# Performance work log

Hardware: AMD Instinct MI355X
Metric: run time of the kernel (lower is better)

## Reference

```python
import jax, jax.numpy as jnp
import numpy as np

B, L, D = 16, 1024, 512
MAX_LEN = 1024  # module hardcodes self.max_len = 1024


def setup_inputs() -> dict:
    key = jax.random.key(0)
    k0, k1, k2, k3, k4 = jax.random.split(key, 5)
    s = 1.0 / np.sqrt(D)
    return {
        "x": jax.random.normal(k0, (B, L, D), jnp.float32),
        "generator": 0.02 * jax.random.normal(k1, (D, 2 * MAX_LEN - 1), jnp.float32),
        "Wq": jax.random.normal(k2, (D, D), jnp.float32) * s,
        "Wv": jax.random.normal(k3, (D, D), jnp.float32) * s,
        "Wc": jax.random.normal(k4, (D, D), jnp.float32) * s,
    }


def reference(x, generator, Wq, Wv, Wc):
    Bc, Lc, Dc = x.shape
    q = x @ Wq.T                      # (B, L, D)
    v = x @ Wv.T                      # (B, L, D)
    # extract_center_window: window of size 2L-1 centered at MAX_LEN-1
    center_full = (generator.shape[-1] + 1) // 2  # == MAX_LEN
    gen = generator[:, center_full - Lc: center_full + Lc - 1]  # (D, 2L-1)
    w = jnp.einsum('bld,di->bli', q, gen)  # (B, L, 2L-1)
    # Toeplitz gather: out[b, l, i] = w[b, l, (L-1) - l + i]
    r = jnp.arange(Lc)
    idx = (Lc - 1) - r[:, None] + r[None, :]  # (L, L)
    w = jnp.take_along_axis(w, idx[None, :, :], axis=-1)  # (B, L, L)
    w = jnp.cumsum(w, axis=1)
    w = jax.nn.relu(w)
    w = jnp.tril(w)
    w = w / (jnp.sum(w, axis=-1, keepdims=True) + 1e-8)
    out = jnp.einsum('bli,bid->bld', w, v)  # (B, L, D)
    return out @ Wc.T
```

## Files before the change

kernel.cpp:

```cpp
#include <hip/hip_runtime.h>
#include <hip/hip_bf16.h>

typedef __attribute__((ext_vector_type(8))) __bf16 bf16x8;
typedef __attribute__((ext_vector_type(4))) __bf16 bf16x4;
typedef __attribute__((ext_vector_type(4))) float  f32x4;

__device__ __forceinline__ void gl_lds16(const __bf16* g, __bf16* l) {
  __builtin_amdgcn_global_load_lds(
      (const __attribute__((address_space(1))) void*)g,
      (__attribute__((address_space(3))) void*)l,
      16, 0, 0);
}


__global__ __launch_bounds__(256) void prep_kernel(
    const float* __restrict__ x, const float* __restrict__ gen,
    const float* __restrict__ Wq, const float* __restrict__ Wv, const float* __restrict__ Wc,
    __bf16* __restrict__ xb, __bf16* __restrict__ genT,
    __bf16* __restrict__ wqT, __bf16* __restrict__ wvT, __bf16* __restrict__ wcb,
    float* __restrict__ gp) {
  __shared__ float S[64][65];
  const int blk = blockIdx.x, tid = threadIdx.x;

  if (blk < 128) {
    const float* in = (blk < 64) ? Wq : Wv;
    __bf16* out = (blk < 64) ? wqT : wvT;
    int t = blk & 63;
    int tx = tid & 63, ty = tid >> 6;
    int d0 = (t >> 3) * 64, e0 = (t & 7) * 64;
#pragma unroll
    for (int i = 0; i < 16; ++i) {
      int di = i * 4 + ty;
      S[di][tx] = in[(long)(d0 + di) * 512 + e0 + tx];
    }
    __syncthreads();
#pragma unroll
    for (int i = 0; i < 16; ++i) {
      int ei = i * 4 + ty;
      out[(long)(e0 + ei) * 512 + d0 + tx] = (__bf16)S[tx][ei];
    }
  } else if (blk < 384) {
    int i = (blk - 128) * 256 + tid;
    float4 v = ((const float4*)Wc)[i];
    bf16x4 o;
    o[0] = (__bf16)v.x; o[1] = (__bf16)v.y; o[2] = (__bf16)v.z; o[3] = (__bf16)v.w;
    *(bf16x4*)(wcb + 4L * i) = o;
  } else if (blk < 2432) {
    int i = blk - 384;
    for (int d = tid; d < 512; d += 256) {
      float v = (i < 2047) ? gen[(long)d * 2047 + i] : 0.f;
      genT[(long)i * 512 + d] = (__bf16)v;
    }
  } else if (blk < 10624) {
    int i = (blk - 2432) * 256 + tid;
    float4 v = ((const float4*)x)[i];
    bf16x4 o;
    o[0] = (__bf16)v.x; o[1] = (__bf16)v.y; o[2] = (__bf16)v.z; o[3] = (__bf16)v.w;
    *(bf16x4*)(xb + 4L * i) = o;
  } else {
    int t = blk - 10624;
    int i = t % 63, c = t / 63;
    int d0 = c * 64, k = tid;
    float a0 = 0.f, a1 = 0.f;
#pragma unroll 8
    for (int u = 0; u < 64; ++u) {
      int d = d0 + u;
      float g = gen[(long)d * 2047 + 992 + i];
      a0 += Wq[(long)d * 512 + k] * g;
      a1 += Wq[(long)d * 512 + k + 256] * g;
    }
    long o = ((long)c * 63 + i) * 512;
    gp[o + k] = a0;
    gp[o + k + 256] = a1;
  }
}

__device__ __forceinline__ void gemm128_body(
    const __bf16* __restrict__ Ab, const __bf16* __restrict__ Bb,
    __bf16 (*As)[128 * 32], __bf16 (*Bs)[128 * 32],
    int m0, int n0, int K, int nt, f32x4 (&acc)[4][4]) {
  const int tid = threadIdx.x;
  const int w = tid >> 6, l = tid & 63;
  const int srow = w * 16 + (l >> 2);
  const int scol = (((l & 3) ^ ((l >> 3) & 3))) * 8;
  const int wr = (w >> 1) * 64, wc = (w & 1) * 64;
  const int fr = l & 15;
  const int cp = (((l >> 4) ^ ((fr >> 1) & 3))) << 3;

  auto STAGE = [&](int t, int p) {
    const int k0 = t << 5;
    gl_lds16(Ab + (long)(m0 + srow) * K + (k0 + scol),      &As[p][(w * 16) * 32]);
    gl_lds16(Ab + (long)(m0 + 64 + srow) * K + (k0 + scol), &As[p][(64 + w * 16) * 32]);
    gl_lds16(Bb + (long)(n0 + srow) * K + (k0 + scol),      &Bs[p][(w * 16) * 32]);
    gl_lds16(Bb + (long)(n0 + 64 + srow) * K + (k0 + scol), &Bs[p][(64 + w * 16) * 32]);
  };
  STAGE(0, 0);
  if (nt > 1) STAGE(1, 1);
  if (nt > 2) STAGE(2, 2);
  int p = 0;
  for (int t = 0; t < nt; ++t) {
    const int ahead = nt - 1 - t;
    if (ahead >= 2)      asm volatile("s_waitcnt vmcnt(8)\ns_barrier" ::: "memory");
    else if (ahead == 1) asm volatile("s_waitcnt vmcnt(4)\ns_barrier" ::: "memory");
    else                 asm volatile("s_waitcnt vmcnt(0)\ns_barrier" ::: "memory");
    bf16x8 af[4], bg[4];
#pragma unroll
    for (int i = 0; i < 4; ++i) af[i] = *(const bf16x8*)&As[p][(wr + i * 16 + fr) * 32 + cp];
#pragma unroll
    for (int j = 0; j < 4; ++j) bg[j] = *(const bf16x8*)&Bs[p][(wc + j * 16 + fr) * 32 + cp];
    asm volatile("s_waitcnt lgkmcnt(0)\ns_barrier" ::: "memory");
    if (t + 3 < nt) STAGE(t + 3, p);
#pragma unroll
    for (int i = 0; i < 4; ++i)
#pragma unroll
      for (int j = 0; j < 4; ++j)
        acc[i][j] = __builtin_amdgcn_mfma_f32_16x16x32_bf16(af[i], bg[j], acc[i][j], 0, 0, 0);
    p = (p == 2) ? 0 : p + 1;
  }
}

__global__ __launch_bounds__(256) void gemm_fold(
    const __bf16* __restrict__ A1, const __bf16* __restrict__ B1, __bf16* __restrict__ C1,
    const __bf16* __restrict__ A2, const __bf16* __restrict__ B2, __bf16* __restrict__ C2,
    const float* __restrict__ gp, float* __restrict__ g2t) {
  __shared__ __bf16 As[3][128 * 32];
  __shared__ __bf16 Bs[3][128 * 32];
  const int b = blockIdx.x;
  if (b >= 80) {
    int idx = (b - 80) * 256 + threadIdx.x;
    if (idx >= 63 * 512) return;
    float s = 0.f;
#pragma unroll
    for (int c = 0; c < 8; ++c) s += gp[(long)c * 63 * 512 + idx];
    g2t[idx] = s;
    return;
  }
  const __bf16 *Ab, *Bb; __bf16* C; int m0, n0;
  if (b < 16) { Ab = A1; Bb = B1; C = C1; m0 = (b >> 2) * 128; n0 = (b & 3) * 128; }
  else { int t = b - 16; Ab = A2; Bb = B2; C = C2; m0 = (t >> 2) * 128; n0 = (t & 3) * 128; }

  f32x4 acc[4][4] = {};
  gemm128_body(Ab, Bb, As, Bs, m0, n0, 512, 16, acc);

  const int l = threadIdx.x & 63, w = threadIdx.x >> 6;
  const int rbase = m0 + (w >> 1) * 64 + ((l >> 4) << 2);
  const int cbase = n0 + (w & 1) * 64 + (l & 15);
#pragma unroll
  for (int i = 0; i < 4; ++i)
#pragma unroll
    for (int r = 0; r < 4; ++r) {
      long row = rbase + i * 16 + r;
#pragma unroll
      for (int j = 0; j < 4; ++j) C[row * 512 + cbase + j * 16] = (__bf16)acc[i][j][r];
    }
}

__global__ __launch_bounds__(256) void gemm_out(
    const __bf16* __restrict__ A, const __bf16* __restrict__ B, float* __restrict__ Cv,
    const float* __restrict__ aux) {
  __shared__ __bf16 As[3][128 * 32];
  __shared__ __bf16 Bs[3][128 * 32];
  int bid = blockIdx.x;
  int swz = (bid & 7) * 64 + (bid >> 3);
  int xn = swz & 3, tt = swz >> 2;
  int yn = tt & 7, bz = tt >> 3;
  const int m0 = yn * 128, n0 = xn * 128;
  const int K = 1024;
  const __bf16* Ab = A + (long)bz * 1024 * 1024;
  const __bf16* Bb = B + (long)bz * 512 * 1024;
  const int nt = (m0 + 128) >> 5;

  f32x4 acc[4][4] = {};
  gemm128_body(Ab, Bb, As, Bs, m0, n0, K, nt, acc);

  const int l = threadIdx.x & 63, w = threadIdx.x >> 6;
  const int rbase = m0 + (w >> 1) * 64 + ((l >> 4) << 2);
  const int cbase = n0 + (w & 1) * 64 + (l & 15);
  float* C = Cv + (long)bz * 512 * 1024;
  const float* ax = aux + bz * 1024;
#pragma unroll
  for (int i = 0; i < 4; ++i)
#pragma unroll
    for (int r = 0; r < 4; ++r) {
      long row = rbase + i * 16 + r;
      float sc = 1.f / (ax[row] + 1e-8f);
#pragma unroll
      for (int j = 0; j < 4; ++j) C[row * 512 + cbase + j * 16] = acc[i][j][r] * sc;
    }
}

__global__ __launch_bounds__(512) void gemm_x(
    const __bf16* __restrict__ A, const __bf16* __restrict__ Bg,
    const __bf16* __restrict__ Pm, __bf16* __restrict__ S, __bf16* __restrict__ vT) {
  __shared__ __bf16 As[3][256 * 32];
  __shared__ __bf16 Bs[3][128 * 32];
  const int tid = threadIdx.x;
  const int w = tid >> 6, l = tid & 63;

  int wgid = blockIdx.x;
  int swz = (wgid & 7) * 112 + (wgid >> 3);
  int y = swz / 14, xt = swz - y * 14;
  const bool band = (xt < 10);
  const int m0 = y * 256;
  const int n0 = band ? (6 - 2 * (y & 3) + xt) * 128 : (xt - 10) * 128;
  const __bf16* Bb = band ? Bg : Pm;
  const int K = 512;

  const int srow = w * 16 + (l >> 2);
  const int scol = (((l & 3) ^ ((l >> 3) & 3))) * 8;
  const int wr = (w >> 1) * 64;
  const int wc = (w & 1) * 64;
  const int fr = l & 15;
  const int cp = (((l >> 4) ^ ((fr >> 1) & 3))) << 3;

  f32x4 acc[4][4] = {};

  auto STAGE = [&](int t, int p) {
    const int k0 = t << 5;
    gl_lds16(A + (long)(m0 + srow) * K + (k0 + scol),        &As[p][(w * 16) * 32]);
    gl_lds16(A + (long)(m0 + 128 + srow) * K + (k0 + scol),  &As[p][(128 + w * 16) * 32]);
    gl_lds16(Bb + (long)(n0 + srow) * K + (k0 + scol),       &Bs[p][(w * 16) * 32]);
  };

  STAGE(0, 0);
  STAGE(1, 1);
  STAGE(2, 2);

  int p = 0;
  for (int t = 0; t < 16; ++t) {
    const int ahead = 15 - t;
    if (ahead >= 2)      asm volatile("s_waitcnt vmcnt(6)\ns_barrier" ::: "memory");
    else if (ahead == 1) asm volatile("s_waitcnt vmcnt(3)\ns_barrier" ::: "memory");
    else                 asm volatile("s_waitcnt vmcnt(0)\ns_barrier" ::: "memory");
    bf16x8 af[4], bg[4];
#pragma unroll
    for (int i = 0; i < 4; ++i) af[i] = *(const bf16x8*)&As[p][(wr + i * 16 + fr) * 32 + cp];
#pragma unroll
    for (int j = 0; j < 4; ++j) bg[j] = *(const bf16x8*)&Bs[p][(wc + j * 16 + fr) * 32 + cp];
    asm volatile("s_waitcnt lgkmcnt(0)\ns_barrier" ::: "memory");
    if (t + 3 < 16) STAGE(t + 3, p);
#pragma unroll
    for (int i = 0; i < 4; ++i)
#pragma unroll
      for (int j = 0; j < 4; ++j)
        acc[i][j] = __builtin_amdgcn_mfma_f32_16x16x32_bf16(af[i], bg[j], acc[i][j], 0, 0, 0);
    p = (p == 2) ? 0 : p + 1;
  }

  const int rbase = m0 + wr + ((l >> 4) << 2);
  const int cbase = n0 + wc + fr;

  if (band) {
#pragma unroll
    for (int i = 0; i < 4; ++i)
#pragma unroll
      for (int r = 0; r < 4; ++r) {
        int row = rbase + i * 16 + r;
        int lloc = row & 1023;
#pragma unroll
        for (int j = 0; j < 4; ++j) {
          int jj = cbase + j * 16 - 1023 + lloc;
          if ((unsigned)jj < 1024u)
            S[(long)row * 1024 + jj] = (__bf16)acc[i][j][r];
        }
      }
  } else {
#pragma unroll
    for (int i = 0; i < 4; ++i) {
      int gm = rbase + i * 16;
      int bt = gm >> 10, lloc = gm & 1023;
#pragma unroll
      for (int j = 0; j < 4; ++j) {
        bf16x4 pk;
        pk[0] = (__bf16)acc[i][j][0]; pk[1] = (__bf16)acc[i][j][1];
        pk[2] = (__bf16)acc[i][j][2]; pk[3] = (__bf16)acc[i][j][3];
        *(bf16x4*)&vT[((long)bt * 512 + cbase + j * 16) * 1024 + lloc] = pk;
      }
    }
  }
}

__global__ __launch_bounds__(128) void chunk_sums(const __bf16* __restrict__ S,
                                                  float* __restrict__ csum,
                                                  float* __restrict__ rowsum) {
  int j0 = threadIdx.x * 8;
  int c = blockIdx.x, b = blockIdx.y;
  if (c < 8) rowsum[b * 1024 + c * 128 + threadIdx.x] = 0.f;
  const __bf16* Sb = S + (long)b * 1024 * 1024;
  float a[8] = {};
  int l0 = c * 16;
  for (int l = l0; l < l0 + 16; ++l) {
    bf16x8 v = *(const bf16x8*)&Sb[(long)l * 1024 + j0];
#pragma unroll
    for (int k = 0; k < 8; ++k) a[k] += (float)v[k];
  }
  long o = ((long)(b * 64 + c) << 10) + j0;
#pragma unroll
  for (int k = 0; k < 8; ++k) csum[o + k] = a[k];
}

__global__ __launch_bounds__(256) void scan_dots(
    float* __restrict__ csum,
    const float* __restrict__ x, const float* __restrict__ g2t, float* __restrict__ Sg) {
  const int blk = blockIdx.x, tid = threadIdx.x;
  if (blk < 64) {
    int idx = blk * 256 + tid;
    int b = idx >> 10, j = idx & 1023;
    long base = ((long)b * 64 << 10) + j;
    float v[64];
#pragma unroll
    for (int c = 0; c < 64; ++c) v[c] = csum[base + ((long)c << 10)];
    float s = 0.f;
#pragma unroll
    for (int c = 0; c < 64; ++c) { csum[base + ((long)c << 10)] = s; s += v[c]; }
  } else {
    int gid = (blk - 64) * 4 + (tid >> 6);
    int lane = tid & 63;
    int b = gid >> 10, rem = gid & 1023, m = rem >> 5, j = rem & 31;
    const float4* xr = (const float4*)(x + ((long)b * 1024 + m) * 512);
    const float4* gr = (const float4*)(g2t + (long)(31 - m + j) * 512);
    float4 a0 = xr[lane * 2], a1 = xr[lane * 2 + 1];
    float4 c0 = gr[lane * 2], c1 = gr[lane * 2 + 1];
    float s = a0.x * c0.x + a0.y * c0.y + a0.z * c0.z + a0.w * c0.w
            + a1.x * c1.x + a1.y * c1.y + a1.z * c1.z + a1.w * c1.w;
#pragma unroll
    for (int off = 32; off; off >>= 1) s += __shfl_down(s, off);
    if (lane == 0) Sg[gid] = s;
  }
}

__global__ __launch_bounds__(128) void cumsum_relu(const __bf16* __restrict__ S,
                                                   const float* __restrict__ csum,
                                                   const float* __restrict__ Sx,
                                                   __bf16* __restrict__ wrelu,
                                                   float* __restrict__ rowsum) {
  int j0 = threadIdx.x * 8;
  int c = blockIdx.x, b = blockIdx.y;
  const bool exact = (c < 2) && (j0 < 32);
  float run[8];
  if (exact) {
#pragma unroll
    for (int k = 0; k < 8; ++k) run[k] = 0.f;
    for (int m = 0; m < c * 16; ++m)
#pragma unroll
      for (int k = 0; k < 8; ++k) run[k] += Sx[b * 1024 + m * 32 + j0 + k];
  } else {
    long co = ((long)(b * 64 + c) << 10) + j0;
#pragma unroll
    for (int k = 0; k < 8; ++k) run[k] = csum[co + k];
  }
  const __bf16* Sb = S + (long)b * 1024 * 1024;
  __bf16* wr = wrelu + (long)b * 1024 * 1024;
  int l0 = c * 16;
  for (int l = l0; l < l0 + 16; ++l) {
    bf16x8 o;
    float rs = 0.f;
    if (exact) {
#pragma unroll
      for (int k = 0; k < 8; ++k) {
        run[k] += Sx[b * 1024 + l * 32 + j0 + k];
        float val = (j0 + k <= l) ? fmaxf(run[k], 0.f) : 0.f;
        o[k] = (__bf16)val;
        rs += val;
      }
    } else {
      bf16x8 v = *(const bf16x8*)&Sb[(long)l * 1024 + j0];
#pragma unroll
      for (int k = 0; k < 8; ++k) {
        run[k] += (float)v[k];
        float val = (j0 + k <= l) ? fmaxf(run[k], 0.f) : 0.f;
        o[k] = (__bf16)val;
        rs += val;
      }
    }
    if (j0 < (((l >> 7) + 1) << 7))
      *(bf16x8*)&wr[(long)l * 1024 + j0] = o;
#pragma unroll
    for (int off = 32; off; off >>= 1) rs += __shfl_down(rs, off);
    if ((threadIdx.x & 63) == 0 && rs != 0.f) atomicAdd(&rowsum[b * 1024 + l], rs);
  }
}

extern "C" void kernel_launch(void* const* d_in, const int* in_sizes, int n_in,
                              void* d_out, int out_size, void* d_ws, size_t ws_size,
                              hipStream_t stream) {
  const float* x   = (const float*)d_in[0];
  const float* gen = (const float*)d_in[1];
  const float* Wq  = (const float*)d_in[2];
  const float* Wv  = (const float*)d_in[3];
  const float* Wc  = (const float*)d_in[4];

  char* ws = (char*)d_ws;
  __bf16* xb    = (__bf16*)(ws + 0L);
  __bf16* vT    = (__bf16*)(ws + 33554432L);
  __bf16* Smat  = (__bf16*)(ws + 67108864L);
  __bf16* wrelu = (__bf16*)(ws + 134217728L);
  __bf16* genT  = (__bf16*)(ws + 167772160L);
  __bf16* wqT   = (__bf16*)(ws + 169869312L);
  __bf16* wvT   = (__bf16*)(ws + 170393600L);
  __bf16* wcb   = (__bf16*)(ws + 170917888L);
  float*  g2t   = (float*)(ws + 171442176L);
  float*  csum  = (float*)(ws + 16777216L);
  float*  rsum  = (float*)(ws + 16777216L + 4194304L);
  float*  Sbuf  = (float*)(ws + 16777216L + 4259840L);
  __bf16* Pmat  = (__bf16*)(ws + 50331648L);
  __bf16* Bg    = (__bf16*)(ws + 51380224L);
  float*  gp    = (float*)(ws + 58720256L);

  prep_kernel<<<11128, 256, 0, stream>>>(x, gen, Wq, Wv, Wc, xb, genT, wqT, wvT, wcb, gp);

  gemm_fold<<<206, 256, 0, stream>>>(wcb, wvT, Pmat, genT, wqT, Bg, gp, g2t);

  gemm_x<<<896, 512, 0, stream>>>(xb, Bg, Pmat, Smat, vT);

  chunk_sums<<<dim3(64, 16), 128, 0, stream>>>(Smat, csum, rsum);
  scan_dots<<<4160, 256, 0, stream>>>(csum, x, g2t, Sbuf);
  cumsum_relu<<<dim3(64, 16), 128, 0, stream>>>(Smat, csum, Sbuf, wrelu, rsum);

  gemm_out<<<512, 256, 0, stream>>>(wrelu, vT, (float*)d_out, rsum);
}
```

Baseline: 137.8 us.

## Enlarge gemm_x tile to 256x256 with BK=64 double-buffered interleaved staging

Rewrites the gemm_x kernel to use 256x256 output tiles with a K-step of 64 and two LDS buffers instead of 256x128 tiles with K-step 32 and three buffers. The band/Toeplitz tile mapping is adjusted to match, so the grid shrinks from 896 to 448 workgroups. Global-to-LDS loads are split into half-tiles and interleaved with the MFMA sub-phases, and s_setprio is raised around the MFMA blocks. The aim is to raise arithmetic intensity and hide load latency. In exchange it uses much more LDS and more accumulator registers per thread, which lowers occupancy, and the band region may now compute more wasted tiles.

After: 139.3 us. Within noise of the previous version (+1.0%).

```diff
diff --git a/kernel.cpp b/kernel.cpp
--- a/kernel.cpp
+++ b/kernel.cpp
@@ -11,7 +11,6 @@
       (__attribute__((address_space(3))) void*)l,
       16, 0, 0);
 }
-
 
 __global__ __launch_bounds__(256) void prep_kernel(
     const float* __restrict__ x, const float* __restrict__ gen,
@@ -192,67 +191,108 @@
 __global__ __launch_bounds__(512) void gemm_x(
     const __bf16* __restrict__ A, const __bf16* __restrict__ Bg,
     const __bf16* __restrict__ Pm, __bf16* __restrict__ S, __bf16* __restrict__ vT) {
-  __shared__ __bf16 As[3][256 * 32];
-  __shared__ __bf16 Bs[3][128 * 32];
+  __shared__ __bf16 Al[2][256 * 64];
+  __shared__ __bf16 Bl[2][256 * 64];
   const int tid = threadIdx.x;
   const int w = tid >> 6, l = tid & 63;
 
   int wgid = blockIdx.x;
-  int swz = (wgid & 7) * 112 + (wgid >> 3);
-  int y = swz / 14, xt = swz - y * 14;
-  const bool band = (xt < 10);
+  int swz = (wgid & 7) * 56 + (wgid >> 3);
+  int y = swz / 7, xt = swz - y * 7;
+  const bool band = (xt < 5);
   const int m0 = y * 256;
-  const int n0 = band ? (6 - 2 * (y & 3) + xt) * 128 : (xt - 10) * 128;
+  const int n0 = band ? (3 - (y & 3) + xt) * 256 : (xt - 5) * 256;
   const __bf16* Bb = band ? Bg : Pm;
   const int K = 512;
 
-  const int srow = w * 16 + (l >> 2);
-  const int scol = (((l & 3) ^ ((l >> 3) & 3))) * 8;
-  const int wr = (w >> 1) * 64;
-  const int wc = (w & 1) * 64;
-  const int fr = l & 15;
-  const int cp = (((l >> 4) ^ ((fr >> 1) & 3))) << 3;
-
-  f32x4 acc[4][4] = {};
-
-  auto STAGE = [&](int t, int p) {
-    const int k0 = t << 5;
-    gl_lds16(A + (long)(m0 + srow) * K + (k0 + scol),        &As[p][(w * 16) * 32]);
-    gl_lds16(A + (long)(m0 + 128 + srow) * K + (k0 + scol),  &As[p][(128 + w * 16) * 32]);
-    gl_lds16(Bb + (long)(n0 + srow) * K + (k0 + scol),       &Bs[p][(w * 16) * 32]);
+  const int wm = w >> 2, wn = w & 3;
+  const int fr = l & 15, fq = l >> 4;
+  const int srow = tid >> 3;
+  const int scol = ((tid & 7) ^ (srow & 7)) * 8;
+  const int rx = fr & 7;
+
+  const __bf16* Abase = A + (long)m0 * K;
+  const __bf16* Bbase = Bb + (long)n0 * K;
+
+  f32x4 acc[8][4] = {};
+
+  auto STAGE = [&](int kt, int h, int d, bool isB) {
+    const __bf16* src = isB ? Bbase : Abase;
+    __bf16* dst = isB ? &Bl[d][0] : &Al[d][0];
+    const int kc = kt * 64 + scol;
+#pragma unroll
+    for (int q = 0; q < 2; ++q) {
+      const int r0 = h * 128 + q * 64;
+      gl_lds16(src + (long)(r0 + srow) * K + kc, dst + (r0 + w * 8) * 64);
+    }
   };
 
-  STAGE(0, 0);
-  STAGE(1, 1);
-  STAGE(2, 2);
-
-  int p = 0;
-  for (int t = 0; t < 16; ++t) {
-    const int ahead = 15 - t;
-    if (ahead >= 2)      asm volatile("s_waitcnt vmcnt(6)\ns_barrier" ::: "memory");
-    else if (ahead == 1) asm volatile("s_waitcnt vmcnt(3)\ns_barrier" ::: "memory");
-    else                 asm volatile("s_waitcnt vmcnt(0)\ns_barrier" ::: "memory");
-    bf16x8 af[4], bg[4];
-#pragma unroll
-    for (int i = 0; i < 4; ++i) af[i] = *(const bf16x8*)&As[p][(wr + i * 16 + fr) * 32 + cp];
-#pragma unroll
-    for (int j = 0; j < 4; ++j) bg[j] = *(const bf16x8*)&Bs[p][(wc + j * 16 + fr) * 32 + cp];
-    asm volatile("s_waitcnt lgkmcnt(0)\ns_barrier" ::: "memory");
-    if (t + 3 < 16) STAGE(t + 3, p);
-#pragma unroll
-    for (int i = 0; i < 4; ++i)
-#pragma unroll
-      for (int j = 0; j < 4; ++j)
-        acc[i][j] = __builtin_amdgcn_mfma_f32_16x16x32_bf16(af[i], bg[j], acc[i][j], 0, 0, 0);
-    p = (p == 2) ? 0 : p + 1;
-  }
-
-  const int rbase = m0 + wr + ((l >> 4) << 2);
-  const int cbase = n0 + wc + fr;
+  STAGE(0, 0, 0, true);  STAGE(0, 1, 0, true);
+  STAGE(0, 0, 0, false); STAGE(0, 1, 0, false);
+  STAGE(1, 0, 1, true);  STAGE(1, 1, 1, true);
+
+  for (int J = 0; J < 4; ++J) {
+    const bool more = (J < 3);
+#pragma unroll
+    for (int ktl = 0; ktl < 2; ++ktl) {
+      const int d = ktl;
+      bf16x8 bg[4][2];
+#pragma unroll
+      for (int p = 0; p < 4; ++p) {
+        if (ktl == 0) {
+          if (p == 0) STAGE(2 * J + 1, 0, 1, false);
+          else if (p == 1) { STAGE(2 * J + 1, 1, 1, false);
+                             if (more) STAGE(2 * J + 2, 0, 0, true); }
+          else if (p == 2) { if (more) STAGE(2 * J + 2, 1, 0, true); }
+        } else {
+          if (p == 0) { if (more) STAGE(2 * J + 2, 0, 0, false); }
+          else if (p == 1) { if (more) { STAGE(2 * J + 2, 1, 0, false);
+                                         STAGE(2 * J + 3, 0, 1, true); } }
+          else if (p == 2) { if (more) STAGE(2 * J + 3, 1, 1, true); }
+        }
+        if (p == 0) {
+          if (ktl == 1 && J == 3) asm volatile("s_waitcnt vmcnt(0)\ns_barrier" ::: "memory");
+          else                    asm volatile("s_waitcnt vmcnt(6)\ns_barrier" ::: "memory");
+        }
+        if (p == 0) {
+#pragma unroll
+          for (int j = 0; j < 4; ++j)
+#pragma unroll
+            for (int ks = 0; ks < 2; ++ks) {
+              const int rho = (wn >> 1) * 128 + (wn & 1) * 64 + j * 16 + fr;
+              bg[j][ks] = *(const bf16x8*)&Bl[d][rho * 64 + (((ks << 2) + fq) ^ rx) * 8];
+            }
+        }
+        bf16x8 af[2][2];
+#pragma unroll
+        for (int u = 0; u < 2; ++u)
+#pragma unroll
+          for (int ks = 0; ks < 2; ++ks) {
+            const int rho = wm * 128 + (2 * p + u) * 16 + fr;
+            af[u][ks] = *(const bf16x8*)&Al[d][rho * 64 + (((ks << 2) + fq) ^ rx) * 8];
+          }
+        asm volatile("s_waitcnt lgkmcnt(0)" ::: "memory");
+        __builtin_amdgcn_s_setprio(1);
+#pragma unroll
+        for (int u = 0; u < 2; ++u)
+#pragma unroll
+          for (int j = 0; j < 4; ++j)
+#pragma unroll
+            for (int ks = 0; ks < 2; ++ks)
+              acc[2 * p + u][j] = __builtin_amdgcn_mfma_f32_16x16x32_bf16(
+                  af[u][ks], bg[j][ks], acc[2 * p + u][j], 0, 0, 0);
+        __builtin_amdgcn_s_setprio(0);
+        asm volatile("s_barrier" ::: "memory");
+      }
+    }
+  }
+
+  const int rbase = m0 + wm * 128 + (fq << 2);
+  const int cbase = n0 + wn * 64 + fr;
 
   if (band) {
 #pragma unroll
-    for (int i = 0; i < 4; ++i)
+    for (int i = 0; i < 8; ++i)
 #pragma unroll
       for (int r = 0; r < 4; ++r) {
         int row = rbase + i * 16 + r;
@@ -266,7 +306,7 @@
       }
   } else {
 #pragma unroll
-    for (int i = 0; i < 4; ++i) {
+    for (int i = 0; i < 8; ++i) {
       int gm = rbase + i * 16;
       int bt = gm >> 10, lloc = gm & 1023;
 #pragma unroll
@@ -411,7 +451,7 @@
 
   gemm_fold<<<206, 256, 0, stream>>>(wcb, wvT, Pmat, genT, wqT, Bg, gp, g2t);
 
-  gemm_x<<<896, 512, 0, stream>>>(xb, Bg, Pmat, Smat, vT);
+  gemm_x<<<448, 512, 0, stream>>>(xb, Bg, Pmat, Smat, vT);
 
   chunk_sums<<<dim3(64, 16), 128, 0, stream>>>(Smat, csum, rsum);
   scan_dots<<<4160, 256, 0, stream>>>(csum, x, g2t, Sbuf);
```
